# Kernel optimization log

Hardware: AMD Instinct MI355X
Metric: run time of the kernel (lower is better)

Reference implementation:

```python
import jax, jax.numpy as jnp
import numpy as np

NBITS = 8  # num_bits_m1 == num_bits_m2 == 8


def _ste_round(x):
    # straight-through estimator round (gradient = identity)
    return x + jax.lax.stop_gradient(jnp.round(x) - x)


def _pact_quantize(x, clip_val, clip_valn, nbits):
    """PACT-style asymmetric quant-dequant with zero alignment (align_zero=True).

    clamp to [clip_valn, clip_val], affine-quantize to [0, 2^n - 1] with a
    rounded zero point, then dequantize.
    """
    levels = jnp.asarray(2 ** nbits - 1, dtype=x.dtype)
    scale = levels / (clip_val - clip_valn)
    zero_point = _ste_round(-clip_valn * scale)  # align zero to an integer level
    xc = jnp.clip(x, clip_valn, clip_val)
    q = _ste_round(xc * scale + zero_point)
    return (q - zero_point) / scale


def setup_inputs() -> dict:
    key = jax.random.key(0)
    k1, k2 = jax.random.split(key)
    B, H, S, D = 2, 16, 1024, 128
    m1 = jax.random.normal(k1, (B, H, S, D), dtype=jnp.float32)
    m2 = jax.random.normal(k2, (B, H, D, S), dtype=jnp.float32)
    return {
        "m1": m1,
        "m2": m2,
        "m1_clip_val": jnp.asarray(1.0, dtype=jnp.float32),
        "m1_clip_valn": jnp.asarray(-1.0, dtype=jnp.float32),
        "m2_clip_val": jnp.asarray(1.0, dtype=jnp.float32),
        "m2_clip_valn": jnp.asarray(-1.0, dtype=jnp.float32),
    }


def reference(m1, m2, m1_clip_val, m1_clip_valn, m2_clip_val, m2_clip_valn):
    qm1 = _pact_quantize(m1, m1_clip_val, m1_clip_valn, NBITS)
    qm2 = _pact_quantize(m2, m2_clip_val, m2_clip_valn, NBITS)
    # replaceBmm=True path: torch.matmul on [B,H,S,D] x [B,H,D,S]
    return jnp.einsum("bhsd,bhdt->bhst", qm1, qm2)
```

## Files before the change

kernel.cpp:

```cpp
#include <hip/hip_runtime.h>

typedef __attribute__((ext_vector_type(8))) short short8;
typedef __attribute__((ext_vector_type(4))) float floatx4;

__device__ __forceinline__ unsigned short quant_bf16(float x, float cvn, float cv,
                                                     float scale, float zp) {
    float xc = fminf(fmaxf(x, cvn), cv);
    float q  = rintf(xc * scale + zp);
    float v  = q - zp;
    return (unsigned short)(__float_as_uint(v) >> 16);
}

__global__ __launch_bounds__(256) void quant_m1_kernel(
        const float* __restrict__ x, unsigned short* __restrict__ q,
        const float* __restrict__ cvp, const float* __restrict__ cvnp, int n4) {
    int i = blockIdx.x * 256 + threadIdx.x;
    if (i >= n4) return;
    float cv = cvp[0], cvn = cvnp[0];
    float scale = 255.0f / (cv - cvn);
    float zp = rintf(-cvn * scale);
    float4 v = ((const float4*)x)[i];
    ushort4 o;
    o.x = quant_bf16(v.x, cvn, cv, scale, zp);
    o.y = quant_bf16(v.y, cvn, cv, scale, zp);
    o.z = quant_bf16(v.z, cvn, cv, scale, zp);
    o.w = quant_bf16(v.w, cvn, cv, scale, zp);
    ((ushort4*)q)[i] = o;
}

__global__ __launch_bounds__(256) void quant_m2t_kernel(
        const float* __restrict__ x, unsigned short* __restrict__ qt,
        const float* __restrict__ cvp, const float* __restrict__ cvnp) {
    __shared__ unsigned short tile[128][129];
    int batch = blockIdx.y;
    int s0 = blockIdx.x * 128;
    const float* xb = x + (size_t)batch * (128 * 1024);
    unsigned short* qb = qt + (size_t)batch * (1024 * 128);
    float cv = cvp[0], cvn = cvnp[0];
    float scale = 255.0f / (cv - cvn);
    float zp = rintf(-cvn * scale);
    int t = threadIdx.x;
    int c4 = t & 31;
    int dbase = t >> 5;
#pragma unroll
    for (int r = 0; r < 16; ++r) {
        int d = dbase + r * 8;
        float4 v = *(const float4*)(xb + d * 1024 + s0 + c4 * 4);
        tile[d][c4 * 4 + 0] = quant_bf16(v.x, cvn, cv, scale, zp);
        tile[d][c4 * 4 + 1] = quant_bf16(v.y, cvn, cv, scale, zp);
        tile[d][c4 * 4 + 2] = quant_bf16(v.z, cvn, cv, scale, zp);
        tile[d][c4 * 4 + 3] = quant_bf16(v.w, cvn, cv, scale, zp);
    }
    __syncthreads();
    int k8 = t & 15;
    int slb = t >> 4;
#pragma unroll
    for (int r = 0; r < 8; ++r) {
        int sl = slb + r * 16;
        short8 o;
#pragma unroll
        for (int j = 0; j < 8; ++j) o[j] = (short)tile[k8 * 8 + j][sl];
        *(short8*)(qb + (size_t)(s0 + sl) * 128 + k8 * 8) = o;
    }
}

__global__ __launch_bounds__(256, 3) void qbmm_kernel(
        const unsigned short* __restrict__ qA, const unsigned short* __restrict__ qBt,
        float* __restrict__ C,
        const float* __restrict__ cv1p, const float* __restrict__ cvn1p,
        const float* __restrict__ cv2p, const float* __restrict__ cvn2p) {
    int batch = blockIdx.z;
    const unsigned short* A  = qA  + (size_t)batch * (1024 * 128);
    const unsigned short* Bt = qBt + (size_t)batch * (1024 * 128);
    float* Cb = C + (size_t)batch * (1024 * 1024);
    int m0 = blockIdx.y * 128, n0 = blockIdx.x * 128;
    int tid = threadIdx.x;
    int lane = tid & 63, w = tid >> 6;
    int wr = w >> 1, wc = w & 1;
    int row16 = lane & 15, quad = lane >> 4;
    int wm = m0 + wr * 64, wn = n0 + wc * 64;

    floatx4 acc[4][4] = {};

    const short8* Ap[4];
    const short8* Bp[4];
#pragma unroll
    for (int i = 0; i < 4; ++i) {
        Ap[i] = (const short8*)(A  + (size_t)(wm + i * 16 + row16) * 128 + quad * 8);
        Bp[i] = (const short8*)(Bt + (size_t)(wn + i * 16 + row16) * 128 + quad * 8);
    }

#pragma unroll
    for (int kk = 0; kk < 4; ++kk) {
        short8 a[4], b[4];
#pragma unroll
        for (int i = 0; i < 4; ++i) { a[i] = Ap[i][kk * 4]; b[i] = Bp[i][kk * 4]; }
#pragma unroll
        for (int mi = 0; mi < 4; ++mi)
#pragma unroll
            for (int ni = 0; ni < 4; ++ni)
                acc[mi][ni] = __builtin_amdgcn_mfma_f32_16x16x32_bf16(
                    a[mi], b[ni], acc[mi][ni], 0, 0, 0);
    }

    float inv = (cv1p[0] - cvn1p[0]) * (cv2p[0] - cvn2p[0]) * (1.0f / 65025.0f);

#pragma unroll
    for (int mi = 0; mi < 4; ++mi) {
#pragma unroll
        for (int r = 0; r < 4; ++r) {
            int row = wm + mi * 16 + quad * 4 + r;
            float* crow = Cb + (size_t)row * 1024 + wn + row16;
#pragma unroll
            for (int ni = 0; ni < 4; ++ni)
                crow[ni * 16] = acc[mi][ni][r] * inv;
        }
    }
}

extern "C" void kernel_launch(void* const* d_in, const int* in_sizes, int n_in,
                              void* d_out, int out_size, void* d_ws, size_t ws_size,
                              hipStream_t stream) {
    const float* m1   = (const float*)d_in[0];
    const float* m2   = (const float*)d_in[1];
    const float* cv1  = (const float*)d_in[2];
    const float* cvn1 = (const float*)d_in[3];
    const float* cv2  = (const float*)d_in[4];
    const float* cvn2 = (const float*)d_in[5];
    float* out = (float*)d_out;

    unsigned short* qA  = (unsigned short*)d_ws;
    unsigned short* qBt = qA + 4194304;

    quant_m1_kernel<<<4096, 256, 0, stream>>>(m1, qA, cv1, cvn1, 1048576);
    quant_m2t_kernel<<<dim3(8, 32), 256, 0, stream>>>(m2, qBt, cv2, cvn2);
    qbmm_kernel<<<dim3(8, 8, 32), 256, 0, stream>>>(qA, qBt, out,
                                                    cv1, cvn1, cv2, cvn2);
}
```

Measured before the change: 188.2 us.

## Vectorize GEMM output stores via swapped MFMA operands and retile m2 transpose

```diff
diff --git a/kernel.cpp b/kernel.cpp
--- a/kernel.cpp
+++ b/kernel.cpp
@@ -19,52 +19,57 @@
     float cv = cvp[0], cvn = cvnp[0];
     float scale = 255.0f / (cv - cvn);
     float zp = rintf(-cvn * scale);
-    float4 v = ((const float4*)x)[i];
+    floatx4 v = ((const floatx4*)x)[i];
     ushort4 o;
-    o.x = quant_bf16(v.x, cvn, cv, scale, zp);
-    o.y = quant_bf16(v.y, cvn, cv, scale, zp);
-    o.z = quant_bf16(v.z, cvn, cv, scale, zp);
-    o.w = quant_bf16(v.w, cvn, cv, scale, zp);
+    o.x = quant_bf16(v[0], cvn, cv, scale, zp);
+    o.y = quant_bf16(v[1], cvn, cv, scale, zp);
+    o.z = quant_bf16(v[2], cvn, cv, scale, zp);
+    o.w = quant_bf16(v[3], cvn, cv, scale, zp);
     ((ushort4*)q)[i] = o;
 }
 
 __global__ __launch_bounds__(256) void quant_m2t_kernel(
         const float* __restrict__ x, unsigned short* __restrict__ qt,
         const float* __restrict__ cvp, const float* __restrict__ cvnp) {
-    __shared__ unsigned short tile[128][129];
+    __shared__ unsigned short ldsT[64][136];
     int batch = blockIdx.y;
-    int s0 = blockIdx.x * 128;
+    int s0 = blockIdx.x * 64;
     const float* xb = x + (size_t)batch * (128 * 1024);
     unsigned short* qb = qt + (size_t)batch * (1024 * 128);
     float cv = cvp[0], cvn = cvnp[0];
     float scale = 255.0f / (cv - cvn);
     float zp = rintf(-cvn * scale);
     int t = threadIdx.x;
-    int c4 = t & 31;
-    int dbase = t >> 5;
 #pragma unroll
-    for (int r = 0; r < 16; ++r) {
-        int d = dbase + r * 8;
-        float4 v = *(const float4*)(xb + d * 1024 + s0 + c4 * 4);
-        tile[d][c4 * 4 + 0] = quant_bf16(v.x, cvn, cv, scale, zp);
-        tile[d][c4 * 4 + 1] = quant_bf16(v.y, cvn, cv, scale, zp);
-        tile[d][c4 * 4 + 2] = quant_bf16(v.z, cvn, cv, scale, zp);
-        tile[d][c4 * 4 + 3] = quant_bf16(v.w, cvn, cv, scale, zp);
+    for (int r = 0; r < 2; ++r) {
+        int u = t + 256 * r;
+        int su = u & 15;
+        int du = u >> 4;
+        floatx4 v[4];
+#pragma unroll
+        for (int i = 0; i < 4; ++i)
+            v[i] = *(const floatx4*)(xb + (size_t)(du * 4 + i) * 1024 + s0 + su * 4);
+#pragma unroll
+        for (int j = 0; j < 4; ++j) {
+            ushort4 w;
+            w.x = quant_bf16(v[0][j], cvn, cv, scale, zp);
+            w.y = quant_bf16(v[1][j], cvn, cv, scale, zp);
+            w.z = quant_bf16(v[2][j], cvn, cv, scale, zp);
+            w.w = quant_bf16(v[3][j], cvn, cv, scale, zp);
+            *(ushort4*)&ldsT[su * 4 + j][du * 4] = w;
+        }
     }
     __syncthreads();
-    int k8 = t & 15;
-    int slb = t >> 4;
 #pragma unroll
-    for (int r = 0; r < 8; ++r) {
-        int sl = slb + r * 16;
-        short8 o;
-#pragma unroll
-        for (int j = 0; j < 8; ++j) o[j] = (short)tile[k8 * 8 + j][sl];
-        *(short8*)(qb + (size_t)(s0 + sl) * 128 + k8 * 8) = o;
+    for (int r = 0; r < 4; ++r) {
+        int c = t + 256 * r;
+        int sl = c >> 4, k8 = c & 15;
+        *(short8*)(qb + (size_t)(s0 + sl) * 128 + k8 * 8) =
+            *(const short8*)&ldsT[sl][k8 * 8];
     }
 }
 
-__global__ __launch_bounds__(256, 3) void qbmm_kernel(
+__global__ __launch_bounds__(256) void qbmm_kernel(
         const unsigned short* __restrict__ qA, const unsigned short* __restrict__ qBt,
         float* __restrict__ C,
         const float* __restrict__ cv1p, const float* __restrict__ cvn1p,
@@ -100,20 +105,19 @@
 #pragma unroll
             for (int ni = 0; ni < 4; ++ni)
                 acc[mi][ni] = __builtin_amdgcn_mfma_f32_16x16x32_bf16(
-                    a[mi], b[ni], acc[mi][ni], 0, 0, 0);
+                    b[ni], a[mi], acc[mi][ni], 0, 0, 0);
     }
 
     float inv = (cv1p[0] - cvn1p[0]) * (cv2p[0] - cvn2p[0]) * (1.0f / 65025.0f);
 
 #pragma unroll
     for (int mi = 0; mi < 4; ++mi) {
+        int s = wm + mi * 16 + row16;
+        float* crow = Cb + (size_t)s * 1024;
 #pragma unroll
-        for (int r = 0; r < 4; ++r) {
-            int row = wm + mi * 16 + quad * 4 + r;
-            float* crow = Cb + (size_t)row * 1024 + wn + row16;
-#pragma unroll
-            for (int ni = 0; ni < 4; ++ni)
-                crow[ni * 16] = acc[mi][ni][r] * inv;
+        for (int ni = 0; ni < 4; ++ni) {
+            floatx4 o = acc[mi][ni] * inv;
+            *(floatx4*)(crow + wn + ni * 16 + quad * 4) = o;
         }
     }
 }
@@ -133,7 +137,7 @@
     unsigned short* qBt = qA + 4194304;
 
     quant_m1_kernel<<<4096, 256, 0, stream>>>(m1, qA, cv1, cvn1, 1048576);
-    quant_m2t_kernel<<<dim3(8, 32), 256, 0, stream>>>(m2, qBt, cv2, cvn2);
+    quant_m2t_kernel<<<dim3(16, 32), 256, 0, stream>>>(m2, qBt, cv2, cvn2);
     qbmm_kernel<<<dim3(8, 8, 32), 256, 0, stream>>>(qA, qBt, out,
                                                     cv1, cvn1, cv2, cvn2);
 }
```

Result: no change. 191.9 us (+1.9%).
